# Performance work log

Hardware: AMD Instinct MI355X
Metric: run time of the kernel (lower is better)

## Reference

```python
import jax, jax.numpy as jnp
import numpy as np

VOCAB, EMB, HID = 100000, 300, 600
B, S, N = 256, 64, 64
MAX_LEVEL = 3  # depth of the fixed 4-ary tree


def _tree():
    parent = np.zeros(N, np.int32)
    level = np.zeros(N, np.int32)
    for i in range(1, N):
        parent[i] = (i - 1) // 4
        level[i] = level[parent[i]] + 1
    return parent, level


def setup_inputs() -> dict:
    key = jax.random.key(0)
    ks = jax.random.split(key, 16)
    parent, level = _tree()
    E_tab = jax.random.normal(ks[0], (VOCAB, EMB), jnp.float32) * 0.1
    E_tab = E_tab.at[0].set(0.0)  # padding_idx=0
    return dict(
        premise_x=jax.random.randint(ks[1], (B, S), 0, VOCAB),
        hypothesis_x=jax.random.randint(ks[2], (B, S), 0, VOCAB),
        p_word_idx=jax.random.randint(ks[3], (B, N), -1, S),  # -1 => ones vector
        p_rel_id=jax.random.randint(ks[4], (B, N), -1, 4),    # 0..2 transformed, -1/3 identity
        h_word_idx=jax.random.randint(ks[5], (B, N), -1, S),
        h_rel_id=jax.random.randint(ks[6], (B, N), -1, 4),
        parent=jnp.asarray(parent),
        level=jnp.asarray(level),
        E_tab=E_tab,
        W_enc=jax.random.normal(ks[7], (3, EMB, EMB), jnp.float32) * 0.1,
        W0_w=jax.random.normal(ks[8], (HID, 6 * EMB), jnp.float32) * 0.1,
        W0_b=jax.random.normal(ks[9], (HID,), jnp.float32) * 0.1,
        W1_w=jax.random.normal(ks[10], (HID, HID), jnp.float32) * 0.1,
        W1_b=jax.random.normal(ks[11], (HID,), jnp.float32) * 0.1,
        W2_w=jax.random.normal(ks[12], (HID, HID), jnp.float32) * 0.1,
        W2_b=jax.random.normal(ks[13], (HID,), jnp.float32) * 0.1,
        Wout_w=jax.random.normal(ks[14], (3, HID), jnp.float32) * 0.1,
        Wout_b=jax.random.normal(ks[15], (3,), jnp.float32) * 0.1,
    )


def _encode_sg(seq, word_idx, rel_id, parent, level, W_enc):
    # Level-synchronous bottom-up evaluation of: leaf -> word,
    # internal -> relu(word * mean(rel-transformed children)).
    Bn, Nn = word_idx.shape
    Ed = seq.shape[-1]
    idx = jnp.clip(word_idx, 0, None)
    word = jnp.take_along_axis(seq, idx[:, :, None], axis=1)        # [B,N,E]
    word = jnp.where((word_idx == -1)[..., None], 1.0, word)        # word_idx==-1 => ones
    h = word
    pflat = (parent[None, :] + (jnp.arange(Bn) * Nn)[:, None]).reshape(-1)
    for l in range(MAX_LEVEL, 0, -1):
        is_child = jnp.broadcast_to(level[None, :] == l, (Bn, Nn))
        # per-relation linear W_enc[r]: h @ W.T (torch Linear, no bias)
        t_all = jnp.einsum('bne,rfe->bnrf', h, W_enc)               # [B,N,3,E]
        sel = jnp.clip(rel_id, 0, 2)[:, :, None, None]
        t = jnp.take_along_axis(t_all, sel, axis=2)[:, :, 0, :]
        t = jnp.where(((rel_id >= 0) & (rel_id <= 2))[..., None], t, h)
        contrib = jnp.where(is_child[..., None], t, 0.0).reshape(Bn * Nn, Ed)
        sums = jnp.zeros((Bn * Nn, Ed), h.dtype).at[pflat].add(contrib)
        counts = jnp.zeros((Bn * Nn,), h.dtype).at[pflat].add(
            is_child.astype(h.dtype).reshape(-1))
        mean = (sums / jnp.maximum(counts, 1.0)[:, None]).reshape(Bn, Nn, Ed)
        has_child = (counts.reshape(Bn, Nn) > 0)
        h = jnp.where(has_child[..., None], jax.nn.relu(word * mean), h)
    return h[:, 0, :]  # root representation


def reference(premise_x, hypothesis_x, p_word_idx, p_rel_id, h_word_idx, h_rel_id,
              parent, level, E_tab, W_enc, W0_w, W0_b, W1_w, W1_b, W2_w, W2_b,
              Wout_w, Wout_b):
    emb_p = E_tab[premise_x]      # [B,S,E]
    emb_h = E_tab[hypothesis_x]
    p_rep = emb_p.sum(axis=1)
    h_rep = emb_h.sum(axis=1)
    p_sg = _encode_sg(emb_p, p_word_idx, p_rel_id, parent, level, W_enc)
    h_sg = _encode_sg(emb_h, h_word_idx, h_rel_id, parent, level, W_enc)
    x = jnp.concatenate([p_rep, h_rep, p_rep - h_rep, p_rep * h_rep,
                         p_sg - h_sg, p_sg * h_sg], axis=1)  # [B,6E]
    h1 = jax.nn.relu(x @ W0_w.T + W0_b)
    h2 = jax.nn.relu(h1 @ W1_w.T + W1_b)
    h3 = jax.nn.relu(h2 @ W2_w.T + W2_b)
    return h3 @ Wout_w.T + Wout_b  # [B,3]
```

## Files before the change

### kernel.cpp

```cpp
#include <hip/hip_runtime.h>

constexpr int NB = 256;
constexpr int NS = 64;
constexpr int NN = 64;
constexpr int NE = 300;
constexpr int NH = 600;

typedef __attribute__((ext_vector_type(8))) short bf16x8;
typedef __attribute__((ext_vector_type(4))) float f32x4;

constexpr int KT0 = 57;
constexpr int KT1 = 19;
constexpr int NJT = 40;
constexpr int HP  = 640;

constexpr size_t OFF_REP = 0;
constexpr size_t SZ_REP  = (size_t)2*NB*NE;
constexpr size_t OFF_ROOT= OFF_REP + SZ_REP;
constexpr size_t OFF_WBF = OFF_ROOT + SZ_REP;
constexpr size_t SZ_WBF  = (size_t)3*20*10*64*8/2;
constexpr size_t OFF_W0S = OFF_WBF + SZ_WBF;
constexpr size_t SZ_W0S  = (size_t)KT0*NJT*64*8/2;
constexpr size_t OFF_W1S = OFF_W0S + SZ_W0S;
constexpr size_t SZ_W1S  = (size_t)KT1*NJT*64*8/2;
constexpr size_t OFF_W2S = OFF_W1S + SZ_W1S;
constexpr size_t OFF_XSW = OFF_W2S + SZ_W1S;
constexpr size_t SZ_XSW  = (size_t)KT0*16*64*8/2;
constexpr size_t OFF_H1  = OFF_XSW + SZ_XSW;
constexpr size_t SZ_H    = (size_t)NB*HP/2;
constexpr size_t OFF_H2  = OFF_H1 + SZ_H;
constexpr size_t OFF_H3  = OFF_H2 + SZ_H;

__device__ __forceinline__ ushort f2bf(float x) {
  unsigned u = __float_as_uint(x);
  unsigned r = (u + 0x7FFFu + ((u >> 16) & 1u)) >> 16;
  return (ushort)r;
}
__device__ __forceinline__ float bf2f(ushort u) {
  return __uint_as_float(((unsigned)u) << 16);
}

constexpr int NSWZ = 3*20*10*64;
constexpr int N0S  = KT0*NJT*64;
constexpr int N1S  = KT1*NJT*64;
constexpr int SETUP_ITEMS  = NSWZ + N0S + 2*N1S;
constexpr int SETUP_BLOCKS = SETUP_ITEMS/256;

__global__ __launch_bounds__(256)
void k_setup(const float* __restrict__ Wenc, const float* __restrict__ W0,
             const float* __restrict__ W1, const float* __restrict__ W2,
             ushort* __restrict__ Wbf, ushort* __restrict__ W0S,
             ushort* __restrict__ W1S, ushort* __restrict__ W2S) {
  int t = blockIdx.x*256 + threadIdx.x;
  if (t < NSWZ) {
    int lane = t & 63, rest = t >> 6;
    int ksi = rest % 10, rnt = rest / 10, nt = rnt % 20, r = rnt / 20;
    int f = nt*16 + (lane & 15), e0 = ksi*32 + (lane >> 4)*8;
    ushort v[8];
    #pragma unroll
    for (int j = 0; j < 8; j++) {
      int e = e0 + j;
      v[j] = (f < NE && e < NE) ? f2bf(Wenc[((size_t)r*NE + f)*NE + e]) : (ushort)0;
    }
    *reinterpret_cast<int4*>(&Wbf[(size_t)t*8]) = *reinterpret_cast<const int4*>(v);
    return;
  }
  t -= NSWZ;
  const float* W; ushort* D; int K;
  if (t < N0S)              { W = W0; D = W0S; K = 6*NE; }
  else { t -= N0S;
    if (t < N1S)            { W = W1; D = W1S; K = NH; }
    else { t -= N1S;          W = W2; D = W2S; K = NH; } }
  int lane = t & 63, g = t >> 6;
  int jt = g % NJT, kt = g / NJT;
  int j  = jt*16 + (lane & 15);
  int kb = kt*32 + (lane >> 4)*8;
  ushort v[8];
  #pragma unroll
  for (int i = 0; i < 8; i++) {
    int k = kb + i;
    v[i] = (j < NH && k < K) ? f2bf(W[(size_t)j*K + k]) : (ushort)0;
  }
  *reinterpret_cast<int4*>(&D[(size_t)t*8]) = *reinterpret_cast<const int4*>(v);
}

constexpr int TS = 328;

__global__ __launch_bounds__(256)
void k_tree(const int* __restrict__ px, const int* __restrict__ hx,
            const int* __restrict__ pwi, const int* __restrict__ prel,
            const int* __restrict__ hwi, const int* __restrict__ hrel,
            const float* __restrict__ Etab, const ushort* __restrict__ Wbf,
            float* __restrict__ rep, float* __restrict__ root) {
  __shared__ __align__(16) ushort hS[64*TS];
  __shared__ int xsh[64];
  __shared__ int wish[64];
  __shared__ int relsh[64];
  const int sb = blockIdx.x;
  const int s = sb >> 8, b = sb & 255;
  const int tid = threadIdx.x;

  if (tid < 64) xsh[tid] = ((s ? hx : px) + b*NS)[tid];
  else if (tid < 128) wish[tid-64] = ((s ? hwi : pwi) + b*NN)[tid-64];
  else if (tid < 192) relsh[tid-128] = ((s ? hrel : prel) + b*NN)[tid-128];
  __syncthreads();

  for (int e = tid; e < NE; e += 256) {
    float acc = 0.f;
    #pragma unroll 8
    for (int j = 0; j < NS; j++) acc += Etab[(size_t)xsh[j]*NE + e];
    rep[(size_t)sb*NE + e] = acc;
  }
  for (int flat = tid; flat < 64*75; flat += 256) {
    int n = flat / 75, c = flat % 75;
    int w = wish[n];
    float4 v;
    if (w < 0) v = float4{1.f,1.f,1.f,1.f};
    else v = *reinterpret_cast<const float4*>(&Etab[(size_t)xsh[w]*NE + c*4]);
    ushort4 o; o.x = f2bf(v.x); o.y = f2bf(v.y); o.z = f2bf(v.z); o.w = f2bf(v.w);
    *reinterpret_cast<ushort4*>(&hS[n*TS + c*4]) = o;
  }
  for (int z = tid; z < 64*10; z += 256) {
    int row = z / 10, cc = z % 10;
    *reinterpret_cast<unsigned*>(&hS[row*TS + 300 + cc*2]) = 0u;
  }
  __syncthreads();

  const int wave = tid >> 6, lane = tid & 63;
  const int mrow = lane & 15, quad = lane >> 4;

  {
    const int mb0 = 21, mb1 = 37, mb2 = 53;
    bf16x8 af[3][10];
    #pragma unroll
    for (int ks = 0; ks < 10; ks++) {
      af[0][ks] = *reinterpret_cast<const bf16x8*>(&hS[(mb0+mrow)*TS + ks*32 + quad*8]);
      af[1][ks] = *reinterpret_cast<const bf16x8*>(&hS[(mb1+mrow)*TS + ks*32 + quad*8]);
      int r2 = min(mb2+mrow, 63);
      af[2][ks] = *reinterpret_cast<const bf16x8*>(&hS[r2*TS + ks*32 + quad*8]);
    }
    __syncthreads();
    for (int pr = wave; pr < 57; pr += 4) {
      int r = pr / 19, nt = pr % 19;
      const ushort* Wb = &Wbf[(size_t)((r*20 + nt)*10)*64*8];
      f32x4 acc0 = f32x4{0.f,0.f,0.f,0.f};
      f32x4 acc1 = f32x4{0.f,0.f,0.f,0.f};
      f32x4 acc2 = f32x4{0.f,0.f,0.f,0.f};
      #pragma unroll
      for (int ks = 0; ks < 10; ks++) {
        bf16x8 bf = *reinterpret_cast<const bf16x8*>(&Wb[((size_t)ks*64 + lane)*8]);
        acc0 = __builtin_amdgcn_mfma_f32_16x16x32_bf16(af[0][ks], bf, acc0, 0, 0, 0);
        acc1 = __builtin_amdgcn_mfma_f32_16x16x32_bf16(af[1][ks], bf, acc1, 0, 0, 0);
        acc2 = __builtin_amdgcn_mfma_f32_16x16x32_bf16(af[2][ks], bf, acc2, 0, 0, 0);
      }
      int f = nt*16 + mrow;
      if (f < NE) {
        #pragma unroll
        for (int reg = 0; reg < 4; reg++) {
          int m = quad*4 + reg;
          int c0 = mb0 + m, c1 = mb1 + m, c2 = mb2 + m;
          if (relsh[c0] == r) hS[c0*TS + f] = f2bf(acc0[reg]);
          if (relsh[c1] == r) hS[c1*TS + f] = f2bf(acc1[reg]);
          if (c2 < 64 && relsh[c2] == r) hS[c2*TS + f] = f2bf(acc2[reg]);
        }
      }
    }
    __syncthreads();
    for (int f = tid; f < NE; f += 256) {
      #pragma unroll
      for (int p = 5; p <= 15; p++) {
        int nc = (p == 15) ? 3 : 4;
        float sum = 0.f;
        for (int j = 0; j < nc; j++) sum += bf2f(hS[(4*p+1+j)*TS + f]);
        float v = bf2f(hS[p*TS + f]) * sum * (1.0f/(float)nc);
        hS[p*TS + f] = f2bf(v > 0.f ? v : 0.f);
      }
    }
    __syncthreads();
  }
  {
    bf16x8 af[10];
    #pragma unroll
    for (int ks = 0; ks < 10; ks++)
      af[ks] = *reinterpret_cast<const bf16x8*>(&hS[(5+mrow)*TS + ks*32 + quad*8]);
    __syncthreads();
    for (int pr = wave; pr < 57; pr += 4) {
      int r = pr / 19, nt = pr % 19;
      const ushort* Wb = &Wbf[(size_t)((r*20 + nt)*10)*64*8];
      f32x4 acc = f32x4{0.f,0.f,0.f,0.f};
      #pragma unroll
      for (int ks = 0; ks < 10; ks++) {
        bf16x8 bf = *reinterpret_cast<const bf16x8*>(&Wb[((size_t)ks*64 + lane)*8]);
        acc = __builtin_amdgcn_mfma_f32_16x16x32_bf16(af[ks], bf, acc, 0, 0, 0);
      }
      int f = nt*16 + mrow;
      if (f < NE) {
        #pragma unroll
        for (int reg = 0; reg < 4; reg++) {
          int c = 5 + quad*4 + reg;
          if (relsh[c] == r) hS[c*TS + f] = f2bf(acc[reg]);
        }
      }
    }
    __syncthreads();
    for (int f = tid; f < NE; f += 256) {
      #pragma unroll
      for (int p = 1; p <= 4; p++) {
        float sum = 0.f;
        #pragma unroll
        for (int j = 0; j < 4; j++) sum += bf2f(hS[(4*p+1+j)*TS + f]);
        float v = bf2f(hS[p*TS + f]) * sum * 0.25f;
        hS[p*TS + f] = f2bf(v > 0.f ? v : 0.f);
      }
    }
    __syncthreads();
  }
  {
    bool rp0 = (relsh[1]==0)|(relsh[2]==0)|(relsh[3]==0)|(relsh[4]==0);
    bool rp1 = (relsh[1]==1)|(relsh[2]==1)|(relsh[3]==1)|(relsh[4]==1);
    bool rp2 = (relsh[1]==2)|(relsh[2]==2)|(relsh[3]==2)|(relsh[4]==2);
    bf16x8 af[10];
    #pragma unroll
    for (int ks = 0; ks < 10; ks++)
      af[ks] = *reinterpret_cast<const bf16x8*>(&hS[(1+min(mrow,3))*TS + ks*32 + quad*8]);
    __syncthreads();
    for (int pr = wave; pr < 57; pr += 4) {
      int r = pr / 19, nt = pr % 19;
      if ((r==0 && !rp0) || (r==1 && !rp1) || (r==2 && !rp2)) continue;
      const ushort* Wb = &Wbf[(size_t)((r*20 + nt)*10)*64*8];
      f32x4 acc = f32x4{0.f,0.f,0.f,0.f};
      #pragma unroll
      for (int ks = 0; ks < 10; ks++) {
        bf16x8 bf = *reinterpret_cast<const bf16x8*>(&Wb[((size_t)ks*64 + lane)*8]);
        acc = __builtin_amdgcn_mfma_f32_16x16x32_bf16(af[ks], bf, acc, 0, 0, 0);
      }
      int f = nt*16 + mrow;
      if (f < NE) {
        #pragma unroll
        for (int reg = 0; reg < 4; reg++) {
          int m = quad*4 + reg;
          if (m < 4 && relsh[1+m] == r) hS[(1+m)*TS + f] = f2bf(acc[reg]);
        }
      }
    }
    __syncthreads();
    for (int f = tid; f < NE; f += 256) {
      float sum = 0.f;
      #pragma unroll
      for (int c = 1; c <= 4; c++) sum += bf2f(hS[c*TS + f]);
      float v = bf2f(hS[0*TS + f]) * sum * 0.25f;
      root[(size_t)sb*NE + f] = v > 0.f ? v : 0.f;
    }
  }
}

constexpr int FEAT_ITEMS  = KT0*16*64;
constexpr int FEAT_BLOCKS = FEAT_ITEMS/256;

__global__ __launch_bounds__(256)
void k_feat(const float* __restrict__ rep, const float* __restrict__ root,
            ushort* __restrict__ Xsw) {
  int t = blockIdx.x*256 + threadIdx.x;
  int lane = t & 63, g = t >> 6;
  int mt = g % 16, kt = g / 16;
  int b  = mt*16 + (lane & 15);
  int kb = kt*32 + (lane >> 4)*8;
  const float* rp = rep  + (size_t)b*NE;
  const float* rh = rep  + (size_t)(NB+b)*NE;
  const float* tp = root + (size_t)b*NE;
  const float* th = root + (size_t)(NB+b)*NE;
  ushort v[8];
  #pragma unroll
  for (int i = 0; i < 8; i++) {
    int k = kb + i;
    float x = 0.f;
    if (k < 6*NE) {
      int seg = k / NE, e = k - seg*NE;
      switch (seg) {
        case 0:  x = rp[e]; break;
        case 1:  x = rh[e]; break;
        case 2:  x = rp[e] - rh[e]; break;
        case 3:  x = rp[e] * rh[e]; break;
        case 4:  x = tp[e] - th[e]; break;
        default: x = tp[e] * th[e]; break;
      }
    }
    v[i] = f2bf(x);
  }
  *reinterpret_cast<int4*>(&Xsw[(size_t)t*8]) = *reinterpret_cast<const int4*>(v);
}

__global__ __launch_bounds__(256)
void k_fc(const ushort* __restrict__ A, const ushort* __restrict__ Wsw,
          const float* __restrict__ bias, ushort* __restrict__ hout,
          int nkt, int mode) {
  __shared__ __align__(16) float red[4*4*64*4];
  const int tid = threadIdx.x, wv = tid >> 6, lane = tid & 63;
  const int bx = blockIdx.x, by = blockIdx.y;

  f32x4 acc[4];
  #pragma unroll
  for (int q = 0; q < 4; q++) acc[q] = f32x4{0.f,0.f,0.f,0.f};

  for (int kt = wv; kt < nkt; kt += 4) {
    bf16x8 a;
    if (mode == 0)
      a = *reinterpret_cast<const bf16x8*>(&A[(((size_t)kt*16 + bx)*64 + lane)*8]);
    else
      a = *reinterpret_cast<const bf16x8*>(
          &A[(size_t)(bx*16 + (lane & 15))*HP + kt*32 + (lane >> 4)*8]);
    #pragma unroll
    for (int q = 0; q < 4; q++) {
      bf16x8 w = *reinterpret_cast<const bf16x8*>(
          &Wsw[(((size_t)kt*NJT + by*4 + q)*64 + lane)*8]);
      acc[q] = __builtin_amdgcn_mfma_f32_16x16x32_bf16(a, w, acc[q], 0, 0, 0);
    }
  }
  #pragma unroll
  for (int q = 0; q < 4; q++)
    *reinterpret_cast<f32x4*>(&red[(((size_t)q*4 + wv)*64 + lane)*4]) = acc[q];
  __syncthreads();
  f32x4 s{0.f,0.f,0.f,0.f};
  #pragma unroll
  for (int w = 0; w < 4; w++) {
    f32x4 p = *reinterpret_cast<f32x4*>(&red[(((size_t)wv*4 + w)*64 + lane)*4]);
    s[0] += p[0]; s[1] += p[1]; s[2] += p[2]; s[3] += p[3];
  }
  int row0 = bx*16 + (lane >> 4)*4;
  int j = (by*4 + wv)*16 + (lane & 15);
  if (j < 608) {
    float bj = (j < NH) ? bias[j] : 0.f;
    #pragma unroll
    for (int r = 0; r < 4; r++) {
      float v = s[r] + bj;
      v = v > 0.f ? v : 0.f;
      hout[(size_t)(row0 + r)*HP + j] = (j < NH) ? f2bf(v) : (ushort)0;
    }
  }
}

__global__ __launch_bounds__(64)
void k_out(const ushort* __restrict__ h3, const float* __restrict__ Wout,
           const float* __restrict__ bout, float* __restrict__ out) {
  int b = blockIdx.x, tid = threadIdx.x;
  float a0 = 0.f, a1 = 0.f, a2 = 0.f;
  for (int k = tid; k < NH; k += 64) {
    float xv = bf2f(h3[(size_t)b*HP + k]);
    a0 += xv * Wout[k];
    a1 += xv * Wout[NH + k];
    a2 += xv * Wout[2*NH + k];
  }
  #pragma unroll
  for (int off = 32; off > 0; off >>= 1) {
    a0 += __shfl_down(a0, off, 64);
    a1 += __shfl_down(a1, off, 64);
    a2 += __shfl_down(a2, off, 64);
  }
  if (tid == 0) {
    out[b*3 + 0] = a0 + bout[0];
    out[b*3 + 1] = a1 + bout[1];
    out[b*3 + 2] = a2 + bout[2];
  }
}

extern "C" void kernel_launch(void* const* d_in, const int* in_sizes, int n_in,
                              void* d_out, int out_size, void* d_ws, size_t ws_size,
                              hipStream_t stream) {
  const int*   px    = (const int*)d_in[0];
  const int*   hx    = (const int*)d_in[1];
  const int*   pwi   = (const int*)d_in[2];
  const int*   prel  = (const int*)d_in[3];
  const int*   hwi   = (const int*)d_in[4];
  const int*   hrel  = (const int*)d_in[5];
  const float* Etab  = (const float*)d_in[8];
  const float* Wenc  = (const float*)d_in[9];
  const float* W0w   = (const float*)d_in[10];
  const float* W0b   = (const float*)d_in[11];
  const float* W1w   = (const float*)d_in[12];
  const float* W1b   = (const float*)d_in[13];
  const float* W2w   = (const float*)d_in[14];
  const float* W2b   = (const float*)d_in[15];
  const float* Woutw = (const float*)d_in[16];
  const float* Woutb = (const float*)d_in[17];

  float* ws   = (float*)d_ws;
  float*  rep  = ws + OFF_REP;
  float*  root = ws + OFF_ROOT;
  ushort* Wbf  = (ushort*)(ws + OFF_WBF);
  ushort* W0S  = (ushort*)(ws + OFF_W0S);
  ushort* W1S  = (ushort*)(ws + OFF_W1S);
  ushort* W2S  = (ushort*)(ws + OFF_W2S);
  ushort* Xsw  = (ushort*)(ws + OFF_XSW);
  ushort* h1   = (ushort*)(ws + OFF_H1);
  ushort* h2   = (ushort*)(ws + OFF_H2);
  ushort* h3   = (ushort*)(ws + OFF_H3);
  float* outp = (float*)d_out;

  k_setup<<<dim3(SETUP_BLOCKS), dim3(256), 0, stream>>>(
      Wenc, W0w, W1w, W2w, Wbf, W0S, W1S, W2S);
  k_tree<<<dim3(2*NB), dim3(256), 0, stream>>>(
      px, hx, pwi, prel, hwi, hrel, Etab, Wbf, rep, root);
  k_feat<<<dim3(FEAT_BLOCKS), dim3(256), 0, stream>>>(rep, root, Xsw);
  k_fc<<<dim3(16,10), dim3(256), 0, stream>>>(Xsw, W0S, W0b, h1, KT0, 0);
  k_fc<<<dim3(16,10), dim3(256), 0, stream>>>(h1,  W1S, W1b, h2, KT1, 1);
  k_fc<<<dim3(16,10), dim3(256), 0, stream>>>(h2,  W2S, W2b, h3, KT1, 1);
  k_out<<<dim3(NB), dim3(64), 0, stream>>>(h3, Woutw, Woutb, outp);
}
```

Measured before the change: 293.0 us.

## Split per-sample tree kernel into batched level-wise GEMM and parent-combine kernels

Replaces the monolithic per-sample tree kernel, which did small MFMA products against the relation weights inside shared memory, with a prep kernel that writes bf16 word rows to global memory. Each tree level then runs a batched GEMM over all nodes of all samples per relation with 64x64 register tiles, followed by a separate kernel that combines children into parents. The aim is better weight reuse and MFMA utilisation across samples instead of re-streaming weights per sample. In exchange it adds six extra launches and global round-trips of intermediates, and it computes all three relations for every node, dropping the old skip of unused relations at the top level.

```diff
diff --git a/kernel.cpp b/kernel.cpp
--- a/kernel.cpp
+++ b/kernel.cpp
@@ -30,6 +30,9 @@
 constexpr size_t SZ_H    = (size_t)NB*HP/2;
 constexpr size_t OFF_H2  = OFF_H1 + SZ_H;
 constexpr size_t OFF_H3  = OFF_H2 + SZ_H;
+constexpr size_t OFF_WRD = OFF_H3 + SZ_H;
+constexpr size_t SZ_WRD  = (size_t)512*64*320/2;
+constexpr size_t OFF_C   = OFF_WRD + SZ_WRD;
 
 __device__ __forceinline__ ushort f2bf(float x) {
   unsigned u = __float_as_uint(x);
@@ -84,25 +87,19 @@
   *reinterpret_cast<int4*>(&D[(size_t)t*8]) = *reinterpret_cast<const int4*>(v);
 }
 
-constexpr int TS = 328;
-
-__global__ __launch_bounds__(256)
-void k_tree(const int* __restrict__ px, const int* __restrict__ hx,
-            const int* __restrict__ pwi, const int* __restrict__ prel,
-            const int* __restrict__ hwi, const int* __restrict__ hrel,
-            const float* __restrict__ Etab, const ushort* __restrict__ Wbf,
-            float* __restrict__ rep, float* __restrict__ root) {
-  __shared__ __align__(16) ushort hS[64*TS];
+__global__ __launch_bounds__(256)
+void k_prep(const int* __restrict__ px, const int* __restrict__ hx,
+            const int* __restrict__ pwi, const int* __restrict__ hwi,
+            const float* __restrict__ Etab, float* __restrict__ rep,
+            ushort* __restrict__ Wrd) {
   __shared__ int xsh[64];
   __shared__ int wish[64];
-  __shared__ int relsh[64];
   const int sb = blockIdx.x;
   const int s = sb >> 8, b = sb & 255;
   const int tid = threadIdx.x;
 
   if (tid < 64) xsh[tid] = ((s ? hx : px) + b*NS)[tid];
   else if (tid < 128) wish[tid-64] = ((s ? hwi : pwi) + b*NN)[tid-64];
-  else if (tid < 192) relsh[tid-128] = ((s ? hrel : prel) + b*NN)[tid-128];
   __syncthreads();
 
   for (int e = tid; e < NE; e += 256) {
@@ -111,146 +108,118 @@
     for (int j = 0; j < NS; j++) acc += Etab[(size_t)xsh[j]*NE + e];
     rep[(size_t)sb*NE + e] = acc;
   }
-  for (int flat = tid; flat < 64*75; flat += 256) {
-    int n = flat / 75, c = flat % 75;
-    int w = wish[n];
-    float4 v;
-    if (w < 0) v = float4{1.f,1.f,1.f,1.f};
-    else v = *reinterpret_cast<const float4*>(&Etab[(size_t)xsh[w]*NE + c*4]);
-    ushort4 o; o.x = f2bf(v.x); o.y = f2bf(v.y); o.z = f2bf(v.z); o.w = f2bf(v.w);
-    *reinterpret_cast<ushort4*>(&hS[n*TS + c*4]) = o;
-  }
-  for (int z = tid; z < 64*10; z += 256) {
-    int row = z / 10, cc = z % 10;
-    *reinterpret_cast<unsigned*>(&hS[row*TS + 300 + cc*2]) = 0u;
-  }
-  __syncthreads();
-
-  const int wave = tid >> 6, lane = tid & 63;
-  const int mrow = lane & 15, quad = lane >> 4;
-
-  {
-    const int mb0 = 21, mb1 = 37, mb2 = 53;
-    bf16x8 af[3][10];
-    #pragma unroll
-    for (int ks = 0; ks < 10; ks++) {
-      af[0][ks] = *reinterpret_cast<const bf16x8*>(&hS[(mb0+mrow)*TS + ks*32 + quad*8]);
-      af[1][ks] = *reinterpret_cast<const bf16x8*>(&hS[(mb1+mrow)*TS + ks*32 + quad*8]);
-      int r2 = min(mb2+mrow, 63);
-      af[2][ks] = *reinterpret_cast<const bf16x8*>(&hS[r2*TS + ks*32 + quad*8]);
-    }
-    __syncthreads();
-    for (int pr = wave; pr < 57; pr += 4) {
-      int r = pr / 19, nt = pr % 19;
-      const ushort* Wb = &Wbf[(size_t)((r*20 + nt)*10)*64*8];
-      f32x4 acc0 = f32x4{0.f,0.f,0.f,0.f};
-      f32x4 acc1 = f32x4{0.f,0.f,0.f,0.f};
-      f32x4 acc2 = f32x4{0.f,0.f,0.f,0.f};
+  for (int flat = tid; flat < 64*80; flat += 256) {
+    int n = flat / 80, c = flat % 80;
+    ushort4 o;
+    if (c < 75) {
+      int w = wish[n];
+      float4 v;
+      if (w < 0) v = float4{1.f,1.f,1.f,1.f};
+      else v = *reinterpret_cast<const float4*>(&Etab[(size_t)xsh[w]*NE + c*4]);
+      o.x = f2bf(v.x); o.y = f2bf(v.y); o.z = f2bf(v.z); o.w = f2bf(v.w);
+    } else {
+      o = ushort4{0,0,0,0};
+    }
+    *reinterpret_cast<ushort4*>(&Wrd[((size_t)sb*64 + n)*320 + c*4]) = o;
+  }
+}
+
+__global__ __launch_bounds__(256)
+void k_t(const ushort* __restrict__ Wrd, const ushort* __restrict__ Wbf,
+         ushort* __restrict__ C, const int* __restrict__ prel,
+         const int* __restrict__ hrel, int NB0, int CNT) {
+  const int tid = threadIdx.x, wv = tid >> 6, lane = tid & 63;
+  const int r = blockIdx.z, by = blockIdx.y;
+  const int b0 = blockIdx.x*256;
+
+  const ushort* aptr[4];
+  #pragma unroll
+  for (int m = 0; m < 4; m++) {
+    int q = b0 + wv*64 + m*16 + (lane & 15);
+    int sb = q / CNT;
+    int node = NB0 + (q - sb*CNT);
+    aptr[m] = Wrd + ((size_t)sb*64 + node)*320 + ((lane >> 4)*8);
+  }
+  const ushort* wp = Wbf + ((size_t)((r*20 + by*4)*10))*512 + (size_t)lane*8;
+
+  f32x4 acc[4][4];
+  #pragma unroll
+  for (int m = 0; m < 4; m++)
+    #pragma unroll
+    for (int q = 0; q < 4; q++) acc[m][q] = f32x4{0.f,0.f,0.f,0.f};
+
+  for (int kt = 0; kt < 10; kt++) {
+    bf16x8 a[4], w[4];
+    #pragma unroll
+    for (int m = 0; m < 4; m++)
+      a[m] = *reinterpret_cast<const bf16x8*>(aptr[m] + kt*32);
+    #pragma unroll
+    for (int q = 0; q < 4; q++)
+      w[q] = *reinterpret_cast<const bf16x8*>(wp + ((size_t)q*10 + kt)*512);
+    #pragma unroll
+    for (int m = 0; m < 4; m++)
       #pragma unroll
-      for (int ks = 0; ks < 10; ks++) {
-        bf16x8 bf = *reinterpret_cast<const bf16x8*>(&Wb[((size_t)ks*64 + lane)*8]);
-        acc0 = __builtin_amdgcn_mfma_f32_16x16x32_bf16(af[0][ks], bf, acc0, 0, 0, 0);
-        acc1 = __builtin_amdgcn_mfma_f32_16x16x32_bf16(af[1][ks], bf, acc1, 0, 0, 0);
-        acc2 = __builtin_amdgcn_mfma_f32_16x16x32_bf16(af[2][ks], bf, acc2, 0, 0, 0);
+      for (int q = 0; q < 4; q++)
+        acc[m][q] = __builtin_amdgcn_mfma_f32_16x16x32_bf16(a[m], w[q], acc[m][q], 0, 0, 0);
+  }
+
+  int relv[4][4];
+  size_t rowoff[4][4];
+  #pragma unroll
+  for (int m = 0; m < 4; m++)
+    #pragma unroll
+    for (int reg = 0; reg < 4; reg++) {
+      int q = b0 + wv*64 + m*16 + (lane >> 4)*4 + reg;
+      int sb = q / CNT;
+      int node = NB0 + (q - sb*CNT);
+      int s = sb >> 8, bb = sb & 255;
+      relv[m][reg] = (s ? hrel : prel)[bb*64 + node];
+      rowoff[m][reg] = ((size_t)sb*64 + node)*320;
+    }
+  #pragma unroll
+  for (int m = 0; m < 4; m++)
+    #pragma unroll
+    for (int qj = 0; qj < 4; qj++) {
+      int j = (by*4 + qj)*16 + (lane & 15);
+      if (j < NE) {
+        #pragma unroll
+        for (int reg = 0; reg < 4; reg++)
+          if (relv[m][reg] == r) C[rowoff[m][reg] + j] = f2bf(acc[m][qj][reg]);
       }
-      int f = nt*16 + mrow;
-      if (f < NE) {
-        #pragma unroll
-        for (int reg = 0; reg < 4; reg++) {
-          int m = quad*4 + reg;
-          int c0 = mb0 + m, c1 = mb1 + m, c2 = mb2 + m;
-          if (relsh[c0] == r) hS[c0*TS + f] = f2bf(acc0[reg]);
-          if (relsh[c1] == r) hS[c1*TS + f] = f2bf(acc1[reg]);
-          if (c2 < 64 && relsh[c2] == r) hS[c2*TS + f] = f2bf(acc2[reg]);
-        }
-      }
-    }
-    __syncthreads();
-    for (int f = tid; f < NE; f += 256) {
-      #pragma unroll
-      for (int p = 5; p <= 15; p++) {
-        int nc = (p == 15) ? 3 : 4;
-        float sum = 0.f;
-        for (int j = 0; j < nc; j++) sum += bf2f(hS[(4*p+1+j)*TS + f]);
-        float v = bf2f(hS[p*TS + f]) * sum * (1.0f/(float)nc);
-        hS[p*TS + f] = f2bf(v > 0.f ? v : 0.f);
-      }
-    }
-    __syncthreads();
-  }
-  {
-    bf16x8 af[10];
-    #pragma unroll
-    for (int ks = 0; ks < 10; ks++)
-      af[ks] = *reinterpret_cast<const bf16x8*>(&hS[(5+mrow)*TS + ks*32 + quad*8]);
-    __syncthreads();
-    for (int pr = wave; pr < 57; pr += 4) {
-      int r = pr / 19, nt = pr % 19;
-      const ushort* Wb = &Wbf[(size_t)((r*20 + nt)*10)*64*8];
-      f32x4 acc = f32x4{0.f,0.f,0.f,0.f};
-      #pragma unroll
-      for (int ks = 0; ks < 10; ks++) {
-        bf16x8 bf = *reinterpret_cast<const bf16x8*>(&Wb[((size_t)ks*64 + lane)*8]);
-        acc = __builtin_amdgcn_mfma_f32_16x16x32_bf16(af[ks], bf, acc, 0, 0, 0);
-      }
-      int f = nt*16 + mrow;
-      if (f < NE) {
-        #pragma unroll
-        for (int reg = 0; reg < 4; reg++) {
-          int c = 5 + quad*4 + reg;
-          if (relsh[c] == r) hS[c*TS + f] = f2bf(acc[reg]);
-        }
-      }
-    }
-    __syncthreads();
-    for (int f = tid; f < NE; f += 256) {
-      #pragma unroll
-      for (int p = 1; p <= 4; p++) {
-        float sum = 0.f;
-        #pragma unroll
-        for (int j = 0; j < 4; j++) sum += bf2f(hS[(4*p+1+j)*TS + f]);
-        float v = bf2f(hS[p*TS + f]) * sum * 0.25f;
-        hS[p*TS + f] = f2bf(v > 0.f ? v : 0.f);
-      }
-    }
-    __syncthreads();
-  }
-  {
-    bool rp0 = (relsh[1]==0)|(relsh[2]==0)|(relsh[3]==0)|(relsh[4]==0);
-    bool rp1 = (relsh[1]==1)|(relsh[2]==1)|(relsh[3]==1)|(relsh[4]==1);
-    bool rp2 = (relsh[1]==2)|(relsh[2]==2)|(relsh[3]==2)|(relsh[4]==2);
-    bf16x8 af[10];
-    #pragma unroll
-    for (int ks = 0; ks < 10; ks++)
-      af[ks] = *reinterpret_cast<const bf16x8*>(&hS[(1+min(mrow,3))*TS + ks*32 + quad*8]);
-    __syncthreads();
-    for (int pr = wave; pr < 57; pr += 4) {
-      int r = pr / 19, nt = pr % 19;
-      if ((r==0 && !rp0) || (r==1 && !rp1) || (r==2 && !rp2)) continue;
-      const ushort* Wb = &Wbf[(size_t)((r*20 + nt)*10)*64*8];
-      f32x4 acc = f32x4{0.f,0.f,0.f,0.f};
-      #pragma unroll
-      for (int ks = 0; ks < 10; ks++) {
-        bf16x8 bf = *reinterpret_cast<const bf16x8*>(&Wb[((size_t)ks*64 + lane)*8]);
-        acc = __builtin_amdgcn_mfma_f32_16x16x32_bf16(af[ks], bf, acc, 0, 0, 0);
-      }
-      int f = nt*16 + mrow;
-      if (f < NE) {
-        #pragma unroll
-        for (int reg = 0; reg < 4; reg++) {
-          int m = quad*4 + reg;
-          if (m < 4 && relsh[1+m] == r) hS[(1+m)*TS + f] = f2bf(acc[reg]);
-        }
-      }
-    }
-    __syncthreads();
-    for (int f = tid; f < NE; f += 256) {
-      float sum = 0.f;
-      #pragma unroll
-      for (int c = 1; c <= 4; c++) sum += bf2f(hS[c*TS + f]);
-      float v = bf2f(hS[0*TS + f]) * sum * 0.25f;
-      root[(size_t)sb*NE + f] = v > 0.f ? v : 0.f;
-    }
+    }
+}
+
+__global__ __launch_bounds__(256)
+void k_par(ushort* __restrict__ Wrd, const ushort* __restrict__ C,
+           const int* __restrict__ prel, const int* __restrict__ hrel,
+           int P0, int NP, float* __restrict__ root) {
+  int t = blockIdx.x*256 + threadIdx.x;
+  int c4 = t % 75, rest = t / 75;
+  int pi = rest % NP, sb = rest / NP;
+  int p = P0 + pi;
+  int s = sb >> 8, bb = sb & 255;
+  const int* relp = (s ? hrel : prel) + bb*64;
+  int nc = (p == 15) ? 3 : 4;
+  float sum0 = 0.f, sum1 = 0.f, sum2 = 0.f, sum3 = 0.f;
+  for (int j = 0; j < nc; j++) {
+    int c = 4*p + 1 + j;
+    int rl = relp[c];
+    const ushort* src = (rl >= 0 && rl <= 2) ? C : Wrd;
+    ushort4 hv = *reinterpret_cast<const ushort4*>(&src[((size_t)sb*64 + c)*320 + c4*4]);
+    sum0 += bf2f(hv.x); sum1 += bf2f(hv.y); sum2 += bf2f(hv.z); sum3 += bf2f(hv.w);
+  }
+  ushort4 wv = *reinterpret_cast<const ushort4*>(&Wrd[((size_t)sb*64 + p)*320 + c4*4]);
+  float inv = 1.0f/(float)nc;
+  float v0 = bf2f(wv.x)*sum0*inv, v1 = bf2f(wv.y)*sum1*inv;
+  float v2 = bf2f(wv.z)*sum2*inv, v3 = bf2f(wv.w)*sum3*inv;
+  v0 = v0 > 0.f ? v0 : 0.f; v1 = v1 > 0.f ? v1 : 0.f;
+  v2 = v2 > 0.f ? v2 : 0.f; v3 = v3 > 0.f ? v3 : 0.f;
+  if (P0 == 0) {
+    float* rp = &root[(size_t)sb*NE + c4*4];
+    rp[0] = v0; rp[1] = v1; rp[2] = v2; rp[3] = v3;
+  } else {
+    ushort4 o; o.x = f2bf(v0); o.y = f2bf(v1); o.z = f2bf(v2); o.w = f2bf(v3);
+    *reinterpret_cast<ushort4*>(&Wrd[((size_t)sb*64 + p)*320 + c4*4]) = o;
   }
 }
 
@@ -394,15 +363,23 @@
   ushort* h1   = (ushort*)(ws + OFF_H1);
   ushort* h2   = (ushort*)(ws + OFF_H2);
   ushort* h3   = (ushort*)(ws + OFF_H3);
+  ushort* Wrd  = (ushort*)(ws + OFF_WRD);
+  ushort* Cbuf = (ushort*)(ws + OFF_C);
   float* outp = (float*)d_out;
 
-  k_setup<<<dim3(SETUP_BLOCKS), dim3(256), 0, stream>>>(
+  dim3 blk(256);
+  k_setup<<<dim3(SETUP_BLOCKS), blk, 0, stream>>>(
       Wenc, W0w, W1w, W2w, Wbf, W0S, W1S, W2S);
-  k_tree<<<dim3(2*NB), dim3(256), 0, stream>>>(
-      px, hx, pwi, prel, hwi, hrel, Etab, Wbf, rep, root);
-  k_feat<<<dim3(FEAT_BLOCKS), dim3(256), 0, stream>>>(rep, root, Xsw);
-  k_fc<<<dim3(16,10), dim3(256), 0, stream>>>(Xsw, W0S, W0b, h1, KT0, 0);
-  k_fc<<<dim3(16,10), dim3(256), 0, stream>>>(h1,  W1S, W1b, h2, KT1, 1);
-  k_fc<<<dim3(16,10), dim3(256), 0, stream>>>(h2,  W2S, W2b, h3, KT1, 1);
+  k_prep<<<dim3(2*NB), blk, 0, stream>>>(px, hx, pwi, hwi, Etab, rep, Wrd);
+  k_t<<<dim3(86, 5, 3), blk, 0, stream>>>(Wrd, Wbf, Cbuf, prel, hrel, 21, 43);
+  k_par<<<dim3(1650), blk, 0, stream>>>(Wrd, Cbuf, prel, hrel, 5, 11, nullptr);
+  k_t<<<dim3(32, 5, 3), blk, 0, stream>>>(Wrd, Wbf, Cbuf, prel, hrel, 5, 16);
+  k_par<<<dim3(600), blk, 0, stream>>>(Wrd, Cbuf, prel, hrel, 1, 4, nullptr);
+  k_t<<<dim3(8, 5, 3), blk, 0, stream>>>(Wrd, Wbf, Cbuf, prel, hrel, 1, 4);
+  k_par<<<dim3(150), blk, 0, stream>>>(Wrd, Cbuf, prel, hrel, 0, 1, root);
+  k_feat<<<dim3(FEAT_BLOCKS), blk, 0, stream>>>(rep, root, Xsw);
+  k_fc<<<dim3(16,10), blk, 0, stream>>>(Xsw, W0S, W0b, h1, KT0, 0);
+  k_fc<<<dim3(16,10), blk, 0, stream>>>(h1,  W1S, W1b, h2, KT1, 1);
+  k_fc<<<dim3(16,10), blk, 0, stream>>>(h2,  W2S, W2b, h3, KT1, 1);
   k_out<<<dim3(NB), dim3(64), 0, stream>>>(h3, Woutw, Woutb, outp);
 }
```

Measured after the change: 333.4 us. 13.8% more time.
